# Performance work log

Hardware: AMD Instinct MI355X
Metric: run time of the kernel (lower is better)

The kernel has to match this reference:

```python
import jax, jax.numpy as jnp
import numpy as np

HID = 512


def _lstm_params(key, in_dim, hid):
    k = 1.0 / np.sqrt(hid)
    ks = jax.random.split(key, 4)
    W_ih = jax.random.uniform(ks[0], (4 * hid, in_dim), minval=-k, maxval=k)
    W_hh = jax.random.uniform(ks[1], (4 * hid, hid), minval=-k, maxval=k)
    b_ih = jax.random.uniform(ks[2], (4 * hid,), minval=-k, maxval=k)
    b_hh = jax.random.uniform(ks[3], (4 * hid,), minval=-k, maxval=k)
    return W_ih, W_hh, b_ih, b_hh


def _linear_params(key, in_dim, out_dim):
    k = 1.0 / np.sqrt(in_dim)
    k1, k2 = jax.random.split(key)
    W = jax.random.uniform(k1, (out_dim, in_dim), minval=-k, maxval=k)
    b = jax.random.uniform(k2, (out_dim,), minval=-k, maxval=k)
    return W, b


def setup_inputs() -> dict:
    key = jax.random.key(0)
    ks = jax.random.split(key, 8)
    state_action = jax.random.normal(ks[0], (32768, 19), dtype=jnp.float32)
    W_ih1, W_hh1, b_ih1, b_hh1 = _lstm_params(ks[1], 19, HID)
    W_ih2, W_hh2, b_ih2, b_hh2 = _lstm_params(ks[2], 19, HID)
    W_xyz, b_xyz = _linear_params(ks[3], HID, 3)
    W_zeta, b_zeta = _linear_params(ks[4], HID, 3)
    W_uvw, b_uvw = _linear_params(ks[5], HID, 3)
    W_pqr, b_pqr = _linear_params(ks[6], HID, 3)
    return dict(state_action=state_action,
                W_ih1=W_ih1, W_hh1=W_hh1, b_ih1=b_ih1, b_hh1=b_hh1,
                W_ih2=W_ih2, W_hh2=W_hh2, b_ih2=b_ih2, b_hh2=b_hh2,
                W_xyz=W_xyz, b_xyz=b_xyz, W_zeta=W_zeta, b_zeta=b_zeta,
                W_uvw=W_uvw, b_uvw=b_uvw, W_pqr=W_pqr, b_pqr=b_pqr)


def _lstm_step(gates_x, h, c, W_hh, b_hh, hid):
    # torch LSTMCell gate order: input, forget, cell(g), output
    g = gates_x + h @ W_hh.T + b_hh
    i = jax.nn.sigmoid(g[:hid])
    f = jax.nn.sigmoid(g[hid:2 * hid])
    gg = jnp.tanh(g[2 * hid:3 * hid])
    o = jax.nn.sigmoid(g[3 * hid:])
    c_new = f * c + i * gg
    h_new = o * jnp.tanh(c_new)
    return h_new, c_new


def reference(state_action, W_ih1, W_hh1, b_ih1, b_hh1,
              W_ih2, W_hh2, b_ih2, b_hh2,
              W_xyz, b_xyz, W_zeta, b_zeta, W_uvw, b_uvw, W_pqr, b_pqr):
    hid = W_hh1.shape[1]
    # precompute input projections for all timesteps (one big GEMM each)
    gx1 = state_action @ W_ih1.T + b_ih1  # [H, 4*hid]
    gx2 = state_action @ W_ih2.T + b_ih2  # [H, 4*hid]

    def step(carry, gx):
        h1, c1, h2, c2 = carry
        g1, g2 = gx
        h1, c1 = _lstm_step(g1, h1, c1, W_hh1, b_hh1, hid)
        h2, c2 = _lstm_step(g2, h2, c2, W_hh2, b_hh2, hid)
        return (h1, c1, h2, c2), (h1, h2)

    z = jnp.zeros((hid,), dtype=state_action.dtype)
    _, (h1s, h2s) = jax.lax.scan(step, (z, z, z, z), (gx1, gx2))
    xyz = h1s @ W_xyz.T + b_xyz
    zeta = h2s @ W_zeta.T + b_zeta
    uvw = h1s @ W_uvw.T + b_uvw
    pqr = h2s @ W_pqr.T + b_pqr
    # original returns a list of [1,12] tensors; we return the stacked [H,12]
    return jnp.concatenate([xyz, zeta, uvw, pqr], axis=1)
```

## Files before the change

kernel.cpp:

```cpp
#include <hip/hip_runtime.h>

#define T_STEPS 32768
#define THREADS 256
#define NLAUNCH 256
#define D_SLOTS 8

typedef unsigned int uint32;
typedef unsigned long long ull;
typedef unsigned int u32x4 __attribute__((ext_vector_type(4)));
typedef unsigned int u32x2 __attribute__((ext_vector_type(2)));


__device__ inline float fsig(float x) {
    return __builtin_amdgcn_rcpf(1.f + __expf(-x));
}
__device__ inline float ftanh(float x) {
    return 1.f - 2.f * __builtin_amdgcn_rcpf(1.f + __expf(2.f * x));
}
__device__ inline float wred64(float x) {
    x += __shfl_xor(x, 1);  x += __shfl_xor(x, 2);  x += __shfl_xor(x, 4);
    x += __shfl_xor(x, 8);  x += __shfl_xor(x, 16); x += __shfl_xor(x, 32);
    return x;
}

__device__ inline void pollflag(const uint32* p, u32x2& f) {
    asm volatile("global_load_dwordx2 %0, %1, off sc0 nt\n\t"
                 "s_waitcnt vmcnt(0)"
                 : "=v"(f) : "v"(p) : "memory");
}
__device__ inline void poll4x(const ull* p, u32x4& v0, u32x4& v1, u32x4& v2, u32x4& v3) {
    asm volatile("global_load_dwordx4 %0, %4, off sc0 nt\n\t"
                 "global_load_dwordx4 %1, %4, off offset:1024 sc0 nt\n\t"
                 "global_load_dwordx4 %2, %4, off offset:2048 sc0 nt\n\t"
                 "global_load_dwordx4 %3, %4, off offset:3072 sc0 nt\n\t"
                 "s_waitcnt vmcnt(0)"
                 : "=&v"(v0), "=&v"(v1), "=&v"(v2), "=&v"(v3)
                 : "v"(p) : "memory");
}

__device__ inline uint32 a_add(uint32* p, uint32 v) {
    return __hip_atomic_fetch_add(p, v, __ATOMIC_RELAXED, __HIP_MEMORY_SCOPE_AGENT);
}
__device__ inline uint32 a_ld(const uint32* p) {
    return __hip_atomic_load(p, __ATOMIC_RELAXED, __HIP_MEMORY_SCOPE_AGENT);
}
__device__ inline void a_st(uint32* p, uint32 v) {
    __hip_atomic_store(p, v, __ATOMIC_RELAXED, __HIP_MEMORY_SCOPE_AGENT);
}

__global__ __launch_bounds__(THREADS, 1)
void lstm_persistent(const float* __restrict__ sa,
                     const float* __restrict__ W_ih1, const float* __restrict__ W_hh1,
                     const float* __restrict__ b_ih1, const float* __restrict__ b_hh1,
                     const float* __restrict__ W_ih2, const float* __restrict__ W_hh2,
                     const float* __restrict__ b_ih2, const float* __restrict__ b_hh2,
                     const float* __restrict__ W_xyz, const float* __restrict__ b_xyz,
                     const float* __restrict__ W_zeta, const float* __restrict__ b_zeta,
                     const float* __restrict__ W_uvw, const float* __restrict__ b_uvw,
                     const float* __restrict__ W_pqr, const float* __restrict__ b_pqr,
                     float* __restrict__ out, ull* hrot, uint32* ready, uint32* claim)
{
    const int tid  = threadIdx.x;
    const int wv   = tid >> 6;
    const int lane = tid & 63;

    __shared__ int s_lstm, s_w;

    if (tid == 0) {
        uint32 xcc;
        asm volatile("s_getreg_b32 %0, hwreg(HW_REG_XCC_ID)" : "=s"(xcc));
        xcc &= 7;
        uint32* cnt     = claim;
        uint32* rankcnt = claim + 8;
        uint32* grank   = claim + 16;

        int lstm = -1, w = 0;
        uint32 slot = a_add(&cnt[xcc], 1);
        if (slot < 32) {
            w = (int)slot;
            if (slot == 31) {
                uint32 rank = a_add(rankcnt, 1);
                a_st(&grank[xcc], (rank < 2) ? (rank + 1) : 0xFEu);
            }
            uint32 g;
            long spins = 0;
            for (;;) {
                g = a_ld(&grank[xcc]);
                if (g != 0) break;
                if (a_ld(rankcnt) >= 2 && ++spins > 200000) { g = 0xFEu; break; }
            }
            if (g != 0xFEu) lstm = (int)g - 1;
        }
        s_lstm = lstm; s_w = w;
    }
    __syncthreads();
    const int lstm = s_lstm;
    const int w    = s_w;
    if (lstm < 0) return;

    const float* W_ih = lstm ? W_ih2 : W_ih1;
    const float* W_hh = lstm ? W_hh2 : W_hh1;
    const float* b_ih = lstm ? b_ih2 : b_ih1;
    const float* b_hh = lstm ? b_hh2 : b_hh1;
    const float* W_a  = lstm ? W_zeta : W_xyz;
    const float* W_b  = lstm ? W_pqr  : W_uvw;

    ull*    hb  = hrot  + (size_t)lstm * D_SLOTS * 512;
    uint32* rdy = ready + lstm * (D_SLOTS * 128);

    __shared__ __align__(16) float hw_all[4][528];
    __shared__ float wih_lds[64 * 19];
    __shared__ float pj_lds[6 * 512];
    float* hw = hw_all[wv];

    const int r  = lane >> 2;
    const int cb = lane & 3;
    const int gt = r >> 2;
    const int jj = r & 3;
    const int G  = gt * 512 + (w << 4) + (wv << 2) + jj;

    float wa[128];
    {
        const float4* wp4 = (const float4*)(W_hh + (size_t)G * 512 + cb * 128);
        #pragma unroll
        for (int k = 0; k < 32; ++k) {
            float4 t4 = wp4[k];
            asm volatile("v_accvgpr_write_b32 %0, %1" : "=a"(wa[4 * k + 0]) : "v"(t4.x));
            asm volatile("v_accvgpr_write_b32 %0, %1" : "=a"(wa[4 * k + 1]) : "v"(t4.y));
            asm volatile("v_accvgpr_write_b32 %0, %1" : "=a"(wa[4 * k + 2]) : "v"(t4.z));
            asm volatile("v_accvgpr_write_b32 %0, %1" : "=a"(wa[4 * k + 3]) : "v"(t4.w));
        }
    }
    for (int idx = tid; idx < 64 * 19; idx += THREADS) {
        int rr = idx / 19, kk = idx - rr * 19;
        int v2 = rr >> 4, r2 = rr & 15;
        int G2 = (r2 >> 2) * 512 + (w << 4) + (v2 << 2) + (r2 & 3);
        wih_lds[idx] = W_ih[G2 * 19 + kk];
    }
    for (int idx = tid; idx < 6 * 512; idx += THREADS) {
        int o = idx >> 9, c = idx & 511;
        pj_lds[idx] = (o < 3) ? W_a[o * 512 + c] : W_b[(o - 3) * 512 + c];
    }
    const float bsum = b_ih[G] + b_hh[G];

    float ball[16];
    #pragma unroll
    for (int k = 0; k < 16; ++k)
        asm volatile("v_accvgpr_write_b32 %0, %1" : "=a"(ball[k]) : "v"(bsum));

    const int d0 = 2 * (wv - 1);
    float pb0 = 0.f, pb1 = 0.f;
    int   col0 = 0, col1 = 0;
    if (wv >= 1) {
        const float* ba = lstm ? b_zeta : b_xyz;
        const float* bb = lstm ? b_pqr  : b_uvw;
        pb0  = (d0 < 3)     ? ba[d0]     : bb[d0 - 3];
        pb1  = (d0 + 1 < 3) ? ba[d0 + 1] : bb[d0 - 2];
        col0 = (d0 < 3)     ? 3 * lstm + d0       : 6 + 3 * lstm + (d0 - 3);
        col1 = (d0 + 1 < 3) ? 3 * lstm + (d0 + 1) : 6 + 3 * lstm + (d0 - 2);
    }

    float c_reg = 0.0f;
    __syncthreads();

    float sav = (lane < 19) ? sa[lane] : 0.f;

    for (int t = 0; t <= T_STEPS; ++t) {
        if (t == T_STEPS && !(wv >= 1 && ((t - 1) & 31) == w)) break;

        float gxv = bsum;
        if (t < T_STEPS) {
            const int base = (wv * 16 + r) * 19;
            #pragma unroll
            for (int k = 0; k < 19; ++k)
                gxv = fmaf(__shfl(sav, k), wih_lds[base + k], gxv);
        }
        float sav_n = 0.f;
        if (lane < 19 && t + 1 < T_STEPS) sav_n = sa[(size_t)(t + 1) * 19 + lane];

        if (t > 0) {
            const uint32 tag  = (uint32)t;
            const int    slot = (int)((uint32)(t - 1) & (D_SLOTS - 1));
            const uint32* fp  = rdy + slot * 128 + 2 * lane;
            u32x2 f;
            for (;;) {
                pollflag(fp, f);
                if (__all((f.x == tag) && (f.y == tag))) break;
            }
            ull* sp = hb + (size_t)slot * 512 + 2 * lane;
            u32x4 v0, v1, v2, v3;
            for (;;) {
                poll4x(sp, v0, v1, v2, v3);
                if (v0.x == tag && v0.z == tag && v1.x == tag && v1.z == tag &&
                    v2.x == tag && v2.z == tag && v3.x == tag && v3.z == tag) break;
            }
            *(float2*)&hw[      2 * lane] = make_float2(__uint_as_float(v0.y), __uint_as_float(v0.w));
            *(float2*)&hw[132 + 2 * lane] = make_float2(__uint_as_float(v1.y), __uint_as_float(v1.w));
            *(float2*)&hw[264 + 2 * lane] = make_float2(__uint_as_float(v2.y), __uint_as_float(v2.w));
            *(float2*)&hw[396 + 2 * lane] = make_float2(__uint_as_float(v3.y), __uint_as_float(v3.w));
        } else if (t == 0) {
            *(float2*)&hw[      2 * lane] = make_float2(0.f, 0.f);
            *(float2*)&hw[132 + 2 * lane] = make_float2(0.f, 0.f);
            *(float2*)&hw[264 + 2 * lane] = make_float2(0.f, 0.f);
            *(float2*)&hw[396 + 2 * lane] = make_float2(0.f, 0.f);
        }

        if (t < T_STEPS) {
            float part = (cb == 0) ? gxv : 0.f;
            {
                const float4* hp4 = (const float4*)&hw[cb * 132];
                float ax = 0.f, ay = 0.f, az = 0.f, aw2 = 0.f;
                #pragma unroll
                for (int k = 0; k < 32; ++k) {
                    float4 hv = hp4[k];
                    float w0, w1, w2, w3;
                    asm volatile("v_accvgpr_read_b32 %0, %1" : "=v"(w0) : "a"(wa[4 * k + 0]));
                    asm volatile("v_accvgpr_read_b32 %0, %1" : "=v"(w1) : "a"(wa[4 * k + 1]));
                    asm volatile("v_accvgpr_read_b32 %0, %1" : "=v"(w2) : "a"(wa[4 * k + 2]));
                    asm volatile("v_accvgpr_read_b32 %0, %1" : "=v"(w3) : "a"(wa[4 * k + 3]));
                    ax  = fmaf(w0, hv.x, ax);
                    ay  = fmaf(w1, hv.y, ay);
                    az  = fmaf(w2, hv.z, az);
                    aw2 = fmaf(w3, hv.w, aw2);
                }
                part += (ax + ay) + (az + aw2);
            }
            part += __shfl_xor(part, 1);
            part += __shfl_xor(part, 2);

            float act = (gt == 2) ? ftanh(part) : fsig(part);
            float i_v = __shfl(act, 4 * jj);
            float f_v = __shfl(act, 16 + 4 * jj);
            float g_v = __shfl(act, 32 + 4 * jj);
            float o_v = __shfl(act, 48 + 4 * jj);

            float hn = 0.f;
            if (r < 4 && cb == 0) {
                c_reg = f_v * c_reg + i_v * g_v;
                hn    = o_v * ftanh(c_reg);
            }
            {
                const uint32 tag2 = (uint32)(t + 1);
                float h1 = __shfl(hn, 4), h2 = __shfl(hn, 8), h3 = __shfl(hn, 12);
                const int slot_t = (int)((uint32)t & (D_SLOTS - 1));
                if (lane == 0) {
                    ull* p = hb + (size_t)slot_t * 512 + (w << 4) + (wv << 2);
                    u32x4 A, B;
                    A.x = tag2; A.y = __float_as_uint(hn);
                    A.z = tag2; A.w = __float_as_uint(h1);
                    B.x = tag2; B.y = __float_as_uint(h2);
                    B.z = tag2; B.w = __float_as_uint(h3);
                    asm volatile("global_store_dwordx4 %0, %1, off sc0\n\t"
                                 "global_store_dwordx4 %2, %3, off sc0"
                                 :: "v"(p), "v"(A), "v"(p + 2), "v"(B) : "memory");
                    asm volatile("s_waitcnt vmcnt(0)" ::: "memory");
                    uint32* fq = rdy + slot_t * 128 + (w << 2) + wv;
                    asm volatile("global_store_dword %0, %1, off sc0"
                                 :: "v"(fq), "v"(tag2) : "memory");
                }
            }
        }

        if (t > 0 && wv >= 1 && ((t - 1) & 31) == w) {
            float a0 = 0.f, a1 = 0.f;
            #pragma unroll
            for (int m = 0; m < 8; ++m) {
                int c = lane + (m << 6);
                float hv = hw[((c >> 7) * 132) + (c & 127)];
                a0 = fmaf(hv, pj_lds[d0 * 512 + c],       a0);
                a1 = fmaf(hv, pj_lds[(d0 + 1) * 512 + c], a1);
            }
            a0 = wred64(a0); a1 = wred64(a1);
            if (lane == 0) {
                size_t ob = (size_t)(t - 1) * 12;
                out[ob + col0] = a0 + pb0;
                out[ob + col1] = a1 + pb1;
            }
        }
        sav = sav_n;
    }

    if (lstm < -1) {
        float s = 0.f;
        #pragma unroll
        for (int k = 0; k < 16; ++k) {
            float tv;
            asm volatile("v_accvgpr_read_b32 %0, %1" : "=v"(tv) : "a"(ball[k]));
            s += tv;
        }
        ((float*)claim)[31] = s;
    }
}

extern "C" void kernel_launch(void* const* d_in, const int* in_sizes, int n_in,
                              void* d_out, int out_size, void* d_ws, size_t ws_size,
                              hipStream_t stream)
{
    const float* sa    = (const float*)d_in[0];
    const float* W_ih1 = (const float*)d_in[1];
    const float* W_hh1 = (const float*)d_in[2];
    const float* b_ih1 = (const float*)d_in[3];
    const float* b_hh1 = (const float*)d_in[4];
    const float* W_ih2 = (const float*)d_in[5];
    const float* W_hh2 = (const float*)d_in[6];
    const float* b_ih2 = (const float*)d_in[7];
    const float* b_hh2 = (const float*)d_in[8];
    const float* W_xyz = (const float*)d_in[9];
    const float* b_xyz = (const float*)d_in[10];
    const float* W_zeta= (const float*)d_in[11];
    const float* b_zeta= (const float*)d_in[12];
    const float* W_uvw = (const float*)d_in[13];
    const float* b_uvw = (const float*)d_in[14];
    const float* W_pqr = (const float*)d_in[15];
    const float* b_pqr = (const float*)d_in[16];

    float*  out   = (float*)d_out;
    ull*    hrot  = (ull*)d_ws;
    uint32* ready = (uint32*)((char*)d_ws + 65536);
    uint32* claim = (uint32*)((char*)d_ws + 65536 + 8192);

    hipMemsetAsync(d_ws, 0, 65536 + 8192 + 128, stream);

    lstm_persistent<<<NLAUNCH, THREADS, 0, stream>>>(
        sa, W_ih1, W_hh1, b_ih1, b_hh1, W_ih2, W_hh2, b_ih2, b_hh2,
        W_xyz, b_xyz, W_zeta, b_zeta, W_uvw, b_uvw, W_pqr, b_pqr,
        out, hrot, ready, claim);
}
```

Baseline: 78.01 ms.

## Replace ready-flag handshake with tagged-data polling and double-buffered loads

Drops the separate per-slot ready-flag array, so consumers poll the tag-packed h slots directly. Two sets of poll loads are kept in flight alternately, and each quarter of h is copied to LDS as soon as its tags match. Producers write each h value as a single 64-bit atomic store of (tag, value) from the owning lane, replacing the shuffle, the two vector stores, the wait and the flag store. This removes one round-trip of global-memory latency per timestep on the recurrent critical path. The stores use workgroup scope, so cross-workgroup visibility is uncertain; a fallback using atomic read-modify-write loads after many spins guards against stale reads.

```diff
diff --git a/kernel.cpp b/kernel.cpp
--- a/kernel.cpp
+++ b/kernel.cpp
@@ -8,7 +8,6 @@
 typedef unsigned int uint32;
 typedef unsigned long long ull;
 typedef unsigned int u32x4 __attribute__((ext_vector_type(4)));
-typedef unsigned int u32x2 __attribute__((ext_vector_type(2)));
 
 
 __device__ inline float fsig(float x) {
@@ -23,20 +22,17 @@
     return x;
 }
 
-__device__ inline void pollflag(const uint32* p, u32x2& f) {
-    asm volatile("global_load_dwordx2 %0, %1, off sc0 nt\n\t"
-                 "s_waitcnt vmcnt(0)"
-                 : "=v"(f) : "v"(p) : "memory");
-}
-__device__ inline void poll4x(const ull* p, u32x4& v0, u32x4& v1, u32x4& v2, u32x4& v3) {
-    asm volatile("global_load_dwordx4 %0, %4, off sc0 nt\n\t"
-                 "global_load_dwordx4 %1, %4, off offset:1024 sc0 nt\n\t"
-                 "global_load_dwordx4 %2, %4, off offset:2048 sc0 nt\n\t"
-                 "global_load_dwordx4 %3, %4, off offset:3072 sc0 nt\n\t"
-                 "s_waitcnt vmcnt(0)"
-                 : "=&v"(v0), "=&v"(v1), "=&v"(v2), "=&v"(v3)
-                 : "v"(p) : "memory");
-}
+#define POLL_ISSUE(sp, v0, v1, v2, v3)                                       \
+    asm volatile("global_load_dwordx4 %0, %4, off sc0 nt\n\t"                \
+                 "global_load_dwordx4 %1, %4, off offset:1024 sc0 nt\n\t"    \
+                 "global_load_dwordx4 %2, %4, off offset:2048 sc0 nt\n\t"    \
+                 "global_load_dwordx4 %3, %4, off offset:3072 sc0 nt"        \
+                 : "=&v"(v0), "=&v"(v1), "=&v"(v2), "=&v"(v3)                \
+                 : "v"(sp) : "memory")
+
+#define WAIT4()                                                              \
+    do { asm volatile("s_waitcnt vmcnt(4)" ::: "memory");                    \
+         __builtin_amdgcn_sched_barrier(0); } while (0)
 
 __device__ inline uint32 a_add(uint32* p, uint32 v) {
     return __hip_atomic_fetch_add(p, v, __ATOMIC_RELAXED, __HIP_MEMORY_SCOPE_AGENT);
@@ -46,6 +42,9 @@
 }
 __device__ inline void a_st(uint32* p, uint32 v) {
     __hip_atomic_store(p, v, __ATOMIC_RELAXED, __HIP_MEMORY_SCOPE_AGENT);
+}
+__device__ inline ull rescue_rmw(ull* p) {
+    return __hip_atomic_fetch_add(p, 0ull, __ATOMIC_RELAXED, __HIP_MEMORY_SCOPE_AGENT);
 }
 
 __global__ __launch_bounds__(THREADS, 1)
@@ -58,7 +57,7 @@
                      const float* __restrict__ W_zeta, const float* __restrict__ b_zeta,
                      const float* __restrict__ W_uvw, const float* __restrict__ b_uvw,
                      const float* __restrict__ W_pqr, const float* __restrict__ b_pqr,
-                     float* __restrict__ out, ull* hrot, uint32* ready, uint32* claim)
+                     float* __restrict__ out, ull* hrot, uint32* claim)
 {
     const int tid  = threadIdx.x;
     const int wv   = tid >> 6;
@@ -105,8 +104,7 @@
     const float* W_a  = lstm ? W_zeta : W_xyz;
     const float* W_b  = lstm ? W_pqr  : W_uvw;
 
-    ull*    hb  = hrot  + (size_t)lstm * D_SLOTS * 512;
-    uint32* rdy = ready + lstm * (D_SLOTS * 128);
+    ull* hb = hrot + (size_t)lstm * D_SLOTS * 512;
 
     __shared__ __align__(16) float hw_all[4][528];
     __shared__ float wih_lds[64 * 19];
@@ -179,25 +177,98 @@
         if (lane < 19 && t + 1 < T_STEPS) sav_n = sa[(size_t)(t + 1) * 19 + lane];
 
         if (t > 0) {
-            const uint32 tag  = (uint32)t;
-            const int    slot = (int)((uint32)(t - 1) & (D_SLOTS - 1));
-            const uint32* fp  = rdy + slot * 128 + 2 * lane;
-            u32x2 f;
+            ull* sp = hb + (size_t)((uint32)(t - 1) & (D_SLOTS - 1)) * 512 + 2 * lane;
+            const uint32 tag = (uint32)t;
+            u32x4 A0, A1, A2, A3, B0, B1, B2, B3;
+            bool d0c = false, d1c = false, d2c = false, d3c = false;
+            int  spin = 0;
+
+            asm volatile("s_waitcnt vmcnt(0)" ::: "memory");
+            POLL_ISSUE(sp, A0, A1, A2, A3);
             for (;;) {
-                pollflag(fp, f);
-                if (__all((f.x == tag) && (f.y == tag))) break;
-            }
-            ull* sp = hb + (size_t)slot * 512 + 2 * lane;
-            u32x4 v0, v1, v2, v3;
-            for (;;) {
-                poll4x(sp, v0, v1, v2, v3);
-                if (v0.x == tag && v0.z == tag && v1.x == tag && v1.z == tag &&
-                    v2.x == tag && v2.z == tag && v3.x == tag && v3.z == tag) break;
-            }
-            *(float2*)&hw[      2 * lane] = make_float2(__uint_as_float(v0.y), __uint_as_float(v0.w));
-            *(float2*)&hw[132 + 2 * lane] = make_float2(__uint_as_float(v1.y), __uint_as_float(v1.w));
-            *(float2*)&hw[264 + 2 * lane] = make_float2(__uint_as_float(v2.y), __uint_as_float(v2.w));
-            *(float2*)&hw[396 + 2 * lane] = make_float2(__uint_as_float(v3.y), __uint_as_float(v3.w));
+                POLL_ISSUE(sp, B0, B1, B2, B3);
+                WAIT4();
+                if (!d0c && __all(A0.x == tag && A0.z == tag)) {
+                    *(float2*)&hw[      2 * lane] = make_float2(__uint_as_float(A0.y), __uint_as_float(A0.w));
+                    d0c = true;
+                }
+                if (!d1c && __all(A1.x == tag && A1.z == tag)) {
+                    *(float2*)&hw[132 + 2 * lane] = make_float2(__uint_as_float(A1.y), __uint_as_float(A1.w));
+                    d1c = true;
+                }
+                if (!d2c && __all(A2.x == tag && A2.z == tag)) {
+                    *(float2*)&hw[264 + 2 * lane] = make_float2(__uint_as_float(A2.y), __uint_as_float(A2.w));
+                    d2c = true;
+                }
+                if (!d3c && __all(A3.x == tag && A3.z == tag)) {
+                    *(float2*)&hw[396 + 2 * lane] = make_float2(__uint_as_float(A3.y), __uint_as_float(A3.w));
+                    d3c = true;
+                }
+                if (d0c && d1c && d2c && d3c) {
+                    asm volatile("s_waitcnt vmcnt(0)" ::: "memory");
+                    break;
+                }
+                POLL_ISSUE(sp, A0, A1, A2, A3);
+                WAIT4();
+                if (!d0c && __all(B0.x == tag && B0.z == tag)) {
+                    *(float2*)&hw[      2 * lane] = make_float2(__uint_as_float(B0.y), __uint_as_float(B0.w));
+                    d0c = true;
+                }
+                if (!d1c && __all(B1.x == tag && B1.z == tag)) {
+                    *(float2*)&hw[132 + 2 * lane] = make_float2(__uint_as_float(B1.y), __uint_as_float(B1.w));
+                    d1c = true;
+                }
+                if (!d2c && __all(B2.x == tag && B2.z == tag)) {
+                    *(float2*)&hw[264 + 2 * lane] = make_float2(__uint_as_float(B2.y), __uint_as_float(B2.w));
+                    d2c = true;
+                }
+                if (!d3c && __all(B3.x == tag && B3.z == tag)) {
+                    *(float2*)&hw[396 + 2 * lane] = make_float2(__uint_as_float(B3.y), __uint_as_float(B3.w));
+                    d3c = true;
+                }
+                if (d0c && d1c && d2c && d3c) {
+                    asm volatile("s_waitcnt vmcnt(0)" ::: "memory");
+                    break;
+                }
+                if (++spin > 100000) {
+                    asm volatile("s_waitcnt vmcnt(0)" ::: "memory");
+                    while (!(d0c && d1c && d2c && d3c)) {
+                        if (!d0c) {
+                            ull x0 = rescue_rmw(sp),       x1 = rescue_rmw(sp + 1);
+                            if ((uint32)x0 == tag && (uint32)x1 == tag) {
+                                *(float2*)&hw[      2 * lane] = make_float2(
+                                    __uint_as_float((uint32)(x0 >> 32)), __uint_as_float((uint32)(x1 >> 32)));
+                                d0c = true;
+                            }
+                        }
+                        if (!d1c) {
+                            ull x0 = rescue_rmw(sp + 128), x1 = rescue_rmw(sp + 129);
+                            if ((uint32)x0 == tag && (uint32)x1 == tag) {
+                                *(float2*)&hw[132 + 2 * lane] = make_float2(
+                                    __uint_as_float((uint32)(x0 >> 32)), __uint_as_float((uint32)(x1 >> 32)));
+                                d1c = true;
+                            }
+                        }
+                        if (!d2c) {
+                            ull x0 = rescue_rmw(sp + 256), x1 = rescue_rmw(sp + 257);
+                            if ((uint32)x0 == tag && (uint32)x1 == tag) {
+                                *(float2*)&hw[264 + 2 * lane] = make_float2(
+                                    __uint_as_float((uint32)(x0 >> 32)), __uint_as_float((uint32)(x1 >> 32)));
+                                d2c = true;
+                            }
+                        }
+                        if (!d3c) {
+                            ull x0 = rescue_rmw(sp + 384), x1 = rescue_rmw(sp + 385);
+                            if ((uint32)x0 == tag && (uint32)x1 == tag) {
+                                *(float2*)&hw[396 + 2 * lane] = make_float2(
+                                    __uint_as_float((uint32)(x0 >> 32)), __uint_as_float((uint32)(x1 >> 32)));
+                                d3c = true;
+                            }
+                        }
+                    }
+                    break;
+                }
+            }
         } else if (t == 0) {
             *(float2*)&hw[      2 * lane] = make_float2(0.f, 0.f);
             *(float2*)&hw[132 + 2 * lane] = make_float2(0.f, 0.f);
@@ -234,30 +305,13 @@
             float g_v = __shfl(act, 32 + 4 * jj);
             float o_v = __shfl(act, 48 + 4 * jj);
 
-            float hn = 0.f;
             if (r < 4 && cb == 0) {
                 c_reg = f_v * c_reg + i_v * g_v;
-                hn    = o_v * ftanh(c_reg);
-            }
-            {
-                const uint32 tag2 = (uint32)(t + 1);
-                float h1 = __shfl(hn, 4), h2 = __shfl(hn, 8), h3 = __shfl(hn, 12);
-                const int slot_t = (int)((uint32)t & (D_SLOTS - 1));
-                if (lane == 0) {
-                    ull* p = hb + (size_t)slot_t * 512 + (w << 4) + (wv << 2);
-                    u32x4 A, B;
-                    A.x = tag2; A.y = __float_as_uint(hn);
-                    A.z = tag2; A.w = __float_as_uint(h1);
-                    B.x = tag2; B.y = __float_as_uint(h2);
-                    B.z = tag2; B.w = __float_as_uint(h3);
-                    asm volatile("global_store_dwordx4 %0, %1, off sc0\n\t"
-                                 "global_store_dwordx4 %2, %3, off sc0"
-                                 :: "v"(p), "v"(A), "v"(p + 2), "v"(B) : "memory");
-                    asm volatile("s_waitcnt vmcnt(0)" ::: "memory");
-                    uint32* fq = rdy + slot_t * 128 + (w << 2) + wv;
-                    asm volatile("global_store_dword %0, %1, off sc0"
-                                 :: "v"(fq), "v"(tag2) : "memory");
-                }
+                float hn = o_v * ftanh(c_reg);
+                ull pk = ((ull)__float_as_uint(hn) << 32) | (ull)(uint32)(t + 1);
+                __hip_atomic_store(
+                    &hb[(size_t)((uint32)t & (D_SLOTS - 1)) * 512 + (w << 4) + (wv << 2) + r],
+                    pk, __ATOMIC_RELAXED, __HIP_MEMORY_SCOPE_WORKGROUP);
             }
         }
 
@@ -316,13 +370,12 @@
 
     float*  out   = (float*)d_out;
     ull*    hrot  = (ull*)d_ws;
-    uint32* ready = (uint32*)((char*)d_ws + 65536);
-    uint32* claim = (uint32*)((char*)d_ws + 65536 + 8192);
-
-    hipMemsetAsync(d_ws, 0, 65536 + 8192 + 128, stream);
+    uint32* claim = (uint32*)((char*)d_ws + 65536);
+
+    hipMemsetAsync(d_ws, 0, 65536 + 128, stream);
 
     lstm_persistent<<<NLAUNCH, THREADS, 0, stream>>>(
         sa, W_ih1, W_hh1, b_ih1, b_hh1, W_ih2, W_hh2, b_ih2, b_hh2,
         W_xyz, b_xyz, W_zeta, b_zeta, W_uvw, b_uvw, W_pqr, b_pqr,
-        out, hrot, ready, claim);
-}
+        out, hrot, claim);
+}
```

Result: no change. 77.03 ms (-1.3%).
